# Optimization experiments

Hardware: AMD Instinct MI355X
Metric: run time of the kernel (lower is better)

## Reference

```python
import jax, jax.numpy as jnp
import numpy as np

T = 512          # tokens
H = 2048         # hidden_size
E = 256          # n_routed_experts (8 groups x 32)
G = 8            # tucker groups
EPG = 32         # experts per group
K = 6            # top_k
I = 1408         # moe_intermediate_size
R1 = 128         # tucker input rank
R2 = 128         # tucker output rank


def setup_inputs() -> dict:
    key = jax.random.key(0)
    ks = jax.random.split(key, 12)
    s = 0.02
    return {
        "hidden_states": jax.random.normal(ks[0], (T, H), jnp.float32),
        "w_router": jax.random.normal(ks[1], (H, E), jnp.float32) * s,
        # gate_proj Tucker factors: H -> I
        "U_in_gate": jax.random.normal(ks[2], (G, H, R1), jnp.float32) * s,
        "core_gate": jax.random.normal(ks[3], (E, R1, R2), jnp.float32) * s,
        "U_out_gate": jax.random.normal(ks[4], (G, I, R2), jnp.float32) * s,
        # up_proj Tucker factors: H -> I
        "U_in_up": jax.random.normal(ks[5], (G, H, R1), jnp.float32) * s,
        "core_up": jax.random.normal(ks[6], (E, R1, R2), jnp.float32) * s,
        "U_out_up": jax.random.normal(ks[7], (G, I, R2), jnp.float32) * s,
        # down_proj Tucker factors: I -> H
        "U_in_down": jax.random.normal(ks[8], (G, I, R1), jnp.float32) * s,
        "core_down": jax.random.normal(ks[9], (E, R1, R2), jnp.float32) * s,
        "U_out_down": jax.random.normal(ks[10], (G, H, R2), jnp.float32) * s,
    }


def _tucker_apply(x, g, e, U_in, core, U_out):
    """Per-expert Tucker linear: y_t = ((x_t @ U_in[g_t]) @ core[e_t]) @ U_out[g_t].T
    x: [Td, din]; g: [Td] group ids; e: [Td] full expert ids.
    U_in: [G, din, r1]; core: [E, r1, r2]; U_out: [G, dout, r2]."""
    h1 = jnp.einsum('td,gdr->tgr', x, U_in)                       # [Td, G, r1]
    h1 = jnp.take_along_axis(h1, g[:, None, None], axis=1)[:, 0]  # [Td, r1]
    h2 = jnp.einsum('tr,trs->ts', h1, core[e])                    # [Td, r2]
    y = jnp.einsum('ts,gds->tgd', h2, U_out)                      # [Td, G, dout]
    return jnp.take_along_axis(y, g[:, None, None], axis=1)[:, 0]


def reference(hidden_states, w_router, U_in_gate, core_gate, U_out_gate,
              U_in_up, core_up, U_out_up, U_in_down, core_down, U_out_down):
    n_tok, hid = hidden_states.shape
    router_logits = hidden_states @ w_router                          # [T, E]
    probs = jax.nn.softmax(router_logits.astype(jnp.float32), axis=-1)
    routing_weights, selected = jax.lax.top_k(probs, K)               # [T, K]
    routing_weights = routing_weights / routing_weights.sum(-1, keepdims=True)
    routing_weights = routing_weights.astype(hidden_states.dtype)

    xd = jnp.repeat(hidden_states, K, axis=0)                         # [T*K, H]
    e = selected.reshape(-1)                                          # [T*K]
    g = e // EPG                                                      # group ids

    gate_out = _tucker_apply(xd, g, e, U_in_gate, core_gate, U_out_gate)
    up_out = _tucker_apply(xd, g, e, U_in_up, core_up, U_out_up)
    inter = jax.nn.silu(gate_out) * up_out                            # [T*K, I]
    down_out = _tucker_apply(inter, g, e, U_in_down, core_down, U_out_down)

    combined = (down_out.reshape(n_tok, K, hid) * routing_weights[..., None]).sum(axis=1)
    return combined
```

## Files before the change

### kernel.cpp

```cpp
#include <hip/hip_runtime.h>
#include <cmath>
#include <cstdint>

#define TNUM 512
#define HID 2048
#define NEXP 256
#define NGRP 8
#define KTOP 6
#define IDIM 1408
#define RNK 128
#define NPAIR (TNUM*KTOP)
#define NRCAP 3328
#define MAXTILES (NRCAP/32)

typedef _Float16 f16;
typedef f16  f16x8 __attribute__((ext_vector_type(8)));
typedef f16  f16x4 __attribute__((ext_vector_type(4)));
typedef float f32x4 __attribute__((ext_vector_type(4)));
#define MFMA16(a,b,c) __builtin_amdgcn_mfma_f32_16x16x32_f16((a),(b),(c),0,0,0)

static __device__ __forceinline__ float4 ld4(const float* p){ return *reinterpret_cast<const float4*>(p); }
static __device__ __forceinline__ void st4(float* p, float4 v){ *reinterpret_cast<float4*>(p) = v; }
static __device__ __forceinline__ f16x8 ldh8(const f16* p){ return *reinterpret_cast<const f16x8*>(p); }

constexpr size_t A256(size_t x){ return (x + 255) & ~(size_t)255; }
constexpr size_t OFF_SEL    = 0;
constexpr size_t OFF_WT     = A256(OFF_SEL    + (size_t)NPAIR*4);
constexpr size_t OFF_CNT    = A256(OFF_WT     + (size_t)NPAIR*4);
constexpr size_t OFF_ESTART = A256(OFF_CNT    + (size_t)NEXP*4);
constexpr size_t OFF_TG     = A256(OFF_ESTART + (size_t)NEXP*4);
constexpr size_t OFF_HDR    = A256(OFF_TG     + (size_t)MAXTILES*4);
constexpr size_t OFF_ROWT   = A256(OFF_HDR    + 16);
constexpr size_t OFF_POS    = A256(OFF_ROWT   + (size_t)NRCAP*4);
constexpr size_t OFF_BIG    = A256(OFF_POS    + (size_t)NPAIR*4);

constexpr size_t SZ_XH    = (size_t)TNUM*HID*2;
constexpr size_t SZ_UTI   = (size_t)NGRP*RNK*HID*2;
constexpr size_t SZ_H1ALL = (size_t)2*TNUM*NGRP*RNK*2;
constexpr size_t SZ_UO    = (size_t)NGRP*IDIM*RNK*2;
constexpr size_t SZ_UOD   = (size_t)NGRP*HID*RNK*2;
constexpr size_t SZ_WR    = (size_t)NEXP*HID*2;
constexpr size_t SZ_H2    = (size_t)NRCAP*RNK*2;
constexpr size_t SZ_INTER = (size_t)NRCAP*IDIM*2;
constexpr size_t SZ_DOWNO = (size_t)NRCAP*HID*2;

constexpr size_t OFF_XH    = OFF_BIG;
constexpr size_t OFF_XL    = OFF_XH   + SZ_XH;
constexpr size_t OFF_UTIG  = OFF_XL   + SZ_XH;
constexpr size_t OFF_UTIU  = OFF_UTIG + SZ_UTI;
constexpr size_t OFF_H1    = OFF_UTIU + SZ_UTI;
constexpr size_t REG_END   = OFF_H1   + SZ_H1ALL;
constexpr size_t OFF_INTER = OFF_XH;
constexpr size_t OFF_DOWNO = OFF_XH;
constexpr size_t OFF_LPART = OFF_H1;
constexpr size_t OFF_UOG   = REG_END;
constexpr size_t OFF_UOU   = OFF_UOG  + SZ_UO;
constexpr size_t OFF_UTID  = OFF_UOU  + SZ_UO;
constexpr size_t OFF_UOD   = OFF_UTID + SZ_UO;
constexpr size_t OFF_WRH   = OFF_UOD  + SZ_UOD;
constexpr size_t OFF_WRL   = OFF_WRH  + SZ_WR;
constexpr size_t OFF_H2G   = OFF_WRL  + SZ_WR;
constexpr size_t OFF_H2U   = OFF_H2G  + SZ_H2;
constexpr size_t OFF_D1    = OFF_H2U  + SZ_H2;
constexpr size_t OFF_D2    = OFF_D1   + SZ_H2;
constexpr size_t WS_NEED   = OFF_D2   + SZ_H2;
static_assert(OFF_INTER + SZ_INTER <= OFF_H1 + 0*SZ_H1ALL + (OFF_H1-OFF_XH), "inter overlay");
static_assert(OFF_INTER + SZ_INTER <= OFF_UTIU + SZ_UTI, "inter must end before H1");
static_assert(OFF_DOWNO + SZ_DOWNO <= OFF_UOG, "downo overlay must end before persistent tail");

__global__ __launch_bounds__(256) void k_cvt(
    const float* __restrict__ x,   const float* __restrict__ Uog,
    const float* __restrict__ Uou, const float* __restrict__ Uod,
    const float* __restrict__ wr,
    const float* __restrict__ Uig, const float* __restrict__ Uiu, const float* __restrict__ Uid,
    f16* __restrict__ xh, f16* __restrict__ xl,
    f16* __restrict__ uog, f16* __restrict__ uou, f16* __restrict__ uod,
    f16* __restrict__ wh, f16* __restrict__ wl,
    f16* __restrict__ ig, f16* __restrict__ iu, f16* __restrict__ idn,
    int* __restrict__ cnt){
  __shared__ float tile[32][33];
  const int b = blockIdx.x, tid = threadIdx.x;
  if(b < 1024){
    const size_t i = (size_t)b*256 + tid;
    float4 v = ld4(x + i*4);
    f16x4 H, L;
    H[0]=(f16)v.x; L[0]=(f16)(v.x-(float)H[0]);
    H[1]=(f16)v.y; L[1]=(f16)(v.y-(float)H[1]);
    H[2]=(f16)v.z; L[2]=(f16)(v.z-(float)H[2]);
    H[3]=(f16)v.w; L[3]=(f16)(v.w-(float)H[3]);
    *reinterpret_cast<f16x4*>(xh + i*4) = H;
    *reinterpret_cast<f16x4*>(xl + i*4) = L;
    return;
  }
  if(b < 5888){
    const float* in; f16* hi; size_t i;
    if(b < 2432){        in = Uog; hi = uog; i = (size_t)(b-1024)*256 + tid; }
    else if(b < 3840){   in = Uou; hi = uou; i = (size_t)(b-2432)*256 + tid; }
    else {               in = Uod; hi = uod; i = (size_t)(b-3840)*256 + tid; }
    float4 v = ld4(in + i*4);
    f16x4 H;
    H[0]=(f16)(v.x*16.f); H[1]=(f16)(v.y*16.f); H[2]=(f16)(v.z*16.f); H[3]=(f16)(v.w*16.f);
    *reinterpret_cast<f16x4*>(hi + i*4) = H;
    return;
  }
  if(b < 6400){
    const int wb = b - 5888;
    if(wb == 0) cnt[tid] = 0;
    const int c0 = (wb & 7)*32, r0 = (wb >> 3)*32;
    { const int r = tid>>3, c4 = (tid&7)*4;
      float4 v = ld4(wr + (size_t)(r0+r)*NEXP + c0 + c4);
      tile[r][c4]=v.x; tile[r][c4+1]=v.y; tile[r][c4+2]=v.z; tile[r][c4+3]=v.w; }
    __syncthreads();
    { const int c = tid>>3, r4 = (tid&7)*4;
      f16x4 H, L;
      #pragma unroll
      for(int k = 0; k < 4; k++){
        float v = tile[r4+k][c]*16.f;
        H[k] = (f16)v; L[k] = (f16)(v - (float)H[k]);
      }
      const size_t o = (size_t)(c0+c)*HID + r0 + r4;
      *reinterpret_cast<f16x4*>(wh + o) = H;
      *reinterpret_cast<f16x4*>(wl + o) = L; }
    return;
  }
  const int b2 = b - 6400;
  const int cx = b2 & 3, ry = (b2>>2) & 63, z = b2 >> 8;
  const int tensor = z >> 3, g = z & 7;
  const float* in; f16* o; int R;
  if(tensor == 0){ in = Uig; o = ig; R = HID; }
  else if(tensor == 1){ in = Uiu; o = iu; R = HID; }
  else { in = Uid; o = idn; R = IDIM; }
  const int r0 = ry*32, c0 = cx*32;
  if(r0 >= R) return;
  in += (size_t)g*R*RNK; o += (size_t)g*RNK*R;
  { const int r = tid>>3, c4 = (tid&7)*4;
    float4 v = ld4(in + (size_t)(r0+r)*RNK + c0 + c4);
    tile[r][c4]=v.x; tile[r][c4+1]=v.y; tile[r][c4+2]=v.z; tile[r][c4+3]=v.w; }
  __syncthreads();
  { const int c = tid>>3, r4 = (tid&7)*4;
    f16x4 H;
    #pragma unroll
    for(int k = 0; k < 4; k++) H[k] = (f16)(tile[r4+k][c]*16.f);
    *reinterpret_cast<f16x4*>(o + (size_t)(c0+c)*R + r0 + r4) = H; }
}

__global__ __launch_bounds__(256) void k_router_mfma(
    const f16* __restrict__ xh, const f16* __restrict__ xl,
    const f16* __restrict__ wh, const f16* __restrict__ wl,
    float* __restrict__ lpart){
  __shared__ float red[4][32][64];
  const int m = blockIdx.x, ecol = blockIdx.y, kz = blockIdx.z;
  const int tid = threadIdx.x;
  const int wid = tid>>6, lane = tid&63, q = lane>>4, id = lane&15;
  const int r0 = m*32, e0 = ecol*64;
  const int kb = kz*512 + wid*128;
  f32x4 acc[2][4];
  #pragma unroll
  for(int f = 0; f < 2; f++)
    #pragma unroll
    for(int c = 0; c < 4; c++) acc[f][c] = (f32x4){0.f,0.f,0.f,0.f};
  #pragma unroll
  for(int kk = 0; kk < 128; kk += 32){
    const size_t a0 = (size_t)(r0+id)*HID    + kb + kk + q*8;
    const size_t a1 = (size_t)(r0+16+id)*HID + kb + kk + q*8;
    f16x8 ah0 = ldh8(xh + a0), al0 = ldh8(xl + a0);
    f16x8 ah1 = ldh8(xh + a1), al1 = ldh8(xl + a1);
    #pragma unroll
    for(int c = 0; c < 4; c++){
      const size_t bo = (size_t)(e0 + c*16 + id)*HID + kb + kk + q*8;
      f16x8 bh = ldh8(wh + bo);
      f16x8 bl = ldh8(wl + bo);
      acc[0][c] = MFMA16(ah0, bh, acc[0][c]);
      acc[0][c] = MFMA16(ah0, bl, acc[0][c]);
      acc[0][c] = MFMA16(al0, bh, acc[0][c]);
      acc[1][c] = MFMA16(ah1, bh, acc[1][c]);
      acc[1][c] = MFMA16(ah1, bl, acc[1][c]);
      acc[1][c] = MFMA16(al1, bh, acc[1][c]);
    }
  }
  #pragma unroll
  for(int f = 0; f < 2; f++)
    #pragma unroll
    for(int c = 0; c < 4; c++)
      #pragma unroll
      for(int r = 0; r < 4; r++)
        red[wid][f*16 + q*4 + r][c*16 + id] = acc[f][c][r];
  __syncthreads();
  const int row = tid>>3, c8 = (tid&7)*8;
  float o[8];
  #pragma unroll
  for(int j = 0; j < 8; j++)
    o[j] = (red[0][row][c8+j] + red[1][row][c8+j] + red[2][row][c8+j] + red[3][row][c8+j])*0.0625f;
  float* dst = &lpart[((size_t)kz*TNUM + r0 + row)*NEXP + e0 + c8];
  st4(dst,     make_float4(o[0],o[1],o[2],o[3]));
  st4(dst + 4, make_float4(o[4],o[5],o[6],o[7]));
}

__global__ __launch_bounds__(256) void k_topk(const float* __restrict__ lpart,
                                              int* __restrict__ sel,
                                              float* __restrict__ wt,
                                              int* __restrict__ cnt){
  __shared__ float wv[4];
  __shared__ int   wi[4];
  __shared__ float swin[KTOP];
  __shared__ int   iwin[KTOP];
  const int t = blockIdx.x, tid = threadIdx.x;
  const int lane = tid & 63, wid = tid >> 6;
  const size_t base = (size_t)t*NEXP + tid;
  float v = lpart[base] + lpart[base + (size_t)TNUM*NEXP]
          + lpart[base + (size_t)2*TNUM*NEXP] + lpart[base + (size_t)3*TNUM*NEXP];
  for(int k = 0; k < KTOP; k++){
    float cv = v; int ci = tid;
    #pragma unroll
    for(int off = 1; off < 64; off <<= 1){
      float ov = __shfl_xor(cv, off);
      int   oi = __shfl_xor(ci, off);
      if(ov > cv || (ov == cv && oi < ci)){ cv = ov; ci = oi; }
    }
    if(lane == 0){ wv[wid] = cv; wi[wid] = ci; }
    __syncthreads();
    if(tid == 0){
      float bv = wv[0]; int bi = wi[0];
      #pragma unroll
      for(int w2 = 1; w2 < 4; w2++)
        if(wv[w2] > bv || (wv[w2] == bv && wi[w2] < bi)){ bv = wv[w2]; bi = wi[w2]; }
      swin[k] = bv; iwin[k] = bi;
    }
    __syncthreads();
    if(tid == iwin[k]) v = -INFINITY;
  }
  if(tid == 0){
    float mx = swin[0], s = 0.f, ww[KTOP];
    #pragma unroll
    for(int k = 0; k < KTOP; k++){ ww[k] = expf(swin[k]-mx); s += ww[k]; }
    float inv = 1.f/s;
    #pragma unroll
    for(int k = 0; k < KTOP; k++){
      sel[t*KTOP+k] = iwin[k];
      wt[t*KTOP+k]  = ww[k]*inv;
      atomicAdd(&cnt[iwin[k]], 1);
    }
  }
}

__global__ __launch_bounds__(256) void k_meta_scatter(
    const int* __restrict__ cnt, const int* __restrict__ sel,
    int* __restrict__ estart, int* __restrict__ tile_group, int* __restrict__ hdr,
    int* __restrict__ row_t, int* __restrict__ pos_of_pair){
  __shared__ int scnt[256];
  __shared__ int gsum[8];
  __shared__ int g0[9];
  __shared__ int curs[256];
  const int tid = threadIdx.x;
  scnt[tid] = cnt[tid];
  if(tid < 8) gsum[tid] = 0;
  __syncthreads();
  atomicAdd(&gsum[tid>>5], scnt[tid]);
  __syncthreads();
  if(tid == 0){
    int run = 0;
    for(int g = 0; g < 8; g++){ g0[g] = run; run += (gsum[g]+31) & ~31; }
    g0[8] = run; hdr[0] = run>>5; hdr[1] = run;
  }
  __syncthreads();
  int g = tid >> 5, s = g0[g];
  for(int i = (g<<5); i < tid; i++) s += scnt[i];
  estart[tid] = s; curs[tid] = s;
  const int nt = g0[8] >> 5;
  for(int t2 = tid; t2 < MAXTILES; t2 += 256){
    int gg = -1;
    if(t2 < nt){
      for(int g2 = 0; g2 < 8; g2++) if(t2*32 >= g0[g2] && t2*32 < g0[g2+1]) gg = g2;
    }
    tile_group[t2] = gg;
  }
  __syncthreads();
  for(int p = tid; p < NPAIR; p += 256){
    const int e = sel[p];
    const int pos = atomicAdd(&curs[e], 1);
    row_t[pos] = p / KTOP;
    pos_of_pair[p] = pos;
  }
}

__global__ __launch_bounds__(256) void k_mm_stage1(
    const f16* __restrict__ xh,
    const f16* __restrict__ Bg_, const f16* __restrict__ Bu_,
    f16* __restrict__ H1){
  __shared__ float red[4][32][64];
  const int nt = blockIdx.x, m = blockIdx.y;
  const int pu = nt>>4, g = (nt>>1)&7, ch = nt&1;
  const f16* B = (pu ? Bu_ : Bg_) + (size_t)g*RNK*HID + (size_t)ch*64*HID;
  const int tid = threadIdx.x;
  const int wid = tid>>6, lane = tid&63, q = lane>>4, id = lane&15;
  const int kb = wid*512;
  const int r0 = m*32;
  f32x4 acc[2][4];
  #pragma unroll
  for(int f = 0; f < 2; f++)
    #pragma unroll
    for(int c = 0; c < 4; c++) acc[f][c] = (f32x4){0.f,0.f,0.f,0.f};
  #pragma unroll 4
  for(int kk = 0; kk < 512; kk += 32){
    f16x8 a0 = ldh8(xh + (size_t)(r0+id)*HID    + kb + kk + q*8);
    f16x8 a1 = ldh8(xh + (size_t)(r0+16+id)*HID + kb + kk + q*8);
    #pragma unroll
    for(int c = 0; c < 4; c++){
      f16x8 b = ldh8(B + (size_t)(c*16+id)*HID + kb + kk + q*8);
      acc[0][c] = MFMA16(a0, b, acc[0][c]);
      acc[1][c] = MFMA16(a1, b, acc[1][c]);
    }
  }
  #pragma unroll
  for(int f = 0; f < 2; f++)
    #pragma unroll
    for(int c = 0; c < 4; c++)
      #pragma unroll
      for(int r = 0; r < 4; r++)
        red[wid][f*16 + q*4 + r][c*16 + id] = acc[f][c][r];
  __syncthreads();
  f16* out = H1 + (size_t)pu*TNUM*(NGRP*RNK);
  const int row = tid>>3, c8 = (tid&7)*8;
  f16x8 o8;
  #pragma unroll
  for(int j = 0; j < 8; j++)
    o8[j] = (f16)(red[0][row][c8+j] + red[1][row][c8+j] + red[2][row][c8+j] + red[3][row][c8+j]);
  *reinterpret_cast<f16x8*>(&out[(size_t)(r0+row)*(NGRP*RNK) + g*RNK + ch*64 + c8]) = o8;
}

__global__ __launch_bounds__(256) void k_core2(
    const float* __restrict__ Cg, const float* __restrict__ Cu,
    const f16* __restrict__ H1,
    const int* __restrict__ estart, const int* __restrict__ cnt,
    const int* __restrict__ row_t,
    f16* __restrict__ h2g, f16* __restrict__ h2u){
  __shared__ f16 Cs[RNK][RNK+8];
  __shared__ float tile[32][33];
  const int e = blockIdx.x, up = blockIdx.y;
  const int n = cnt[e];
  if(n == 0) return;
  const float* Cf = (up ? Cu : Cg) + (size_t)e*RNK*RNK;
  const int tid = threadIdx.x;
  #pragma unroll 2
  for(int st = 0; st < 16; st++){
    const int R0 = (st>>2)*32, C0 = (st&3)*32;
    { const int r = tid>>3, c4 = (tid&7)*4;
      float4 v = ld4(Cf + (size_t)(R0+r)*RNK + C0 + c4);
      tile[r][c4]=v.x; tile[r][c4+1]=v.y; tile[r][c4+2]=v.z; tile[r][c4+3]=v.w; }
    __syncthreads();
    { const int c = tid>>3, r4 = (tid&7)*4;
      f16x4 H;
      #pragma unroll
      for(int k2 = 0; k2 < 4; k2++) H[k2] = (f16)(tile[r4+k2][c]*16.f);
      *reinterpret_cast<f16x4*>(&Cs[C0+c][R0+r4]) = H; }
    __syncthreads();
  }
  const int j0 = estart[e], g = e >> 5;
  const f16* A = H1 + (size_t)up*TNUM*(NGRP*RNK);
  f16* o = up ? h2u : h2g;
  const int wid = tid>>6, lane = tid&63, q = lane>>4, id = lane&15;
  for(int rt = 0; rt*16 < n; rt++){
    const int jrow = j0 + rt*16 + id;
    const int jj = jrow < j0+n ? jrow : j0;
    const f16* arow = A + (size_t)row_t[jj]*(NGRP*RNK) + g*RNK;
    f32x4 acc0 = (f32x4){0.f,0.f,0.f,0.f};
    f32x4 acc1 = (f32x4){0.f,0.f,0.f,0.f};
    #pragma unroll
    for(int kk = 0; kk < RNK; kk += 32){
      f16x8 a = ldh8(arow + kk + q*8);
      f16x8 b0 = *reinterpret_cast<const f16x8*>(&Cs[wid*32 + id][kk + q*8]);
      f16x8 b1 = *reinterpret_cast<const f16x8*>(&Cs[wid*32 + 16 + id][kk + q*8]);
      acc0 = MFMA16(a, b0, acc0);
      acc1 = MFMA16(a, b1, acc1);
    }
    #pragma unroll
    for(int r = 0; r < 4; r++){
      const int j = j0 + rt*16 + q*4 + r;
      if(j < j0+n){
        o[(size_t)j*RNK + wid*32 + id]      = (f16)acc0[r];
        o[(size_t)j*RNK + wid*32 + 16 + id] = (f16)acc1[r];
      }
    }
  }
}

__global__ __launch_bounds__(128) void k_mm_gateup(
    const f16* __restrict__ Ag, const f16* __restrict__ Au,
    const f16* __restrict__ Bg, const f16* __restrict__ Bu,
    const int* __restrict__ tg,
    f16* __restrict__ inter){
  const int g = tg[blockIdx.x];
  if(g < 0) return;
  const int j0 = blockIdx.x*32;
  const int tid = threadIdx.x;
  const int wid = tid>>6, lane = tid&63, q = lane>>4, id = lane&15;
  const int c0 = blockIdx.y*128 + wid*64;
  const size_t bbase = (size_t)g*IDIM*RNK;
  f32x4 accg[2][4], accu[2][4];
  #pragma unroll
  for(int f = 0; f < 2; f++)
    #pragma unroll
    for(int c = 0; c < 4; c++){ accg[f][c] = (f32x4){0.f,0.f,0.f,0.f}; accu[f][c] = (f32x4){0.f,0.f,0.f,0.f}; }
  #pragma unroll 2
  for(int kk = 0; kk < RNK; kk += 32){
    const size_t a0off = (size_t)(j0+id)*RNK    + kk + q*8;
    const size_t a1off = (size_t)(j0+16+id)*RNK + kk + q*8;
    f16x8 ag0 = ldh8(Ag + a0off), ag1 = ldh8(Ag + a1off);
    f16x8 au0 = ldh8(Au + a0off), au1 = ldh8(Au + a1off);
    #pragma unroll
    for(int c = 0; c < 4; c++){
      const size_t boff = bbase + (size_t)(c0 + c*16 + id)*RNK + kk + q*8;
      f16x8 bg = ldh8(Bg + boff);
      f16x8 bu = ldh8(Bu + boff);
      accg[0][c] = MFMA16(ag0, bg, accg[0][c]);
      accg[1][c] = MFMA16(ag1, bg, accg[1][c]);
      accu[0][c] = MFMA16(au0, bu, accu[0][c]);
      accu[1][c] = MFMA16(au1, bu, accu[1][c]);
    }
  }
  #pragma unroll
  for(int f = 0; f < 2; f++)
    #pragma unroll
    for(int c = 0; c < 4; c++)
      #pragma unroll
      for(int r = 0; r < 4; r++){
        float vg = accg[f][c][r] * (1.f/4096.f);
        float vu = accu[f][c][r] * (1.f/4096.f);
        float sv = vg/(1.f+expf(-vg))*vu*256.f;
        inter[(size_t)(j0 + f*16 + q*4 + r)*IDIM + c0 + c*16 + id] = (f16)sv;
      }
}

__global__ __launch_bounds__(256) void k_mm_down_in(
    const f16* __restrict__ A_, const f16* __restrict__ B_,
    const int* __restrict__ tg,
    f16* __restrict__ d1){
  __shared__ float red[4][32][64];
  const int g = tg[blockIdx.x];
  if(g < 0) return;
  const int j0 = blockIdx.x*32;
  const int ch = blockIdx.y;
  const f16* B = B_ + (size_t)g*RNK*IDIM + (size_t)ch*64*IDIM;
  const int tid = threadIdx.x;
  const int wid = tid>>6, lane = tid&63, q = lane>>4, id = lane&15;
  const int kb = wid*352;
  f32x4 acc[2][4];
  #pragma unroll
  for(int f = 0; f < 2; f++)
    #pragma unroll
    for(int c = 0; c < 4; c++) acc[f][c] = (f32x4){0.f,0.f,0.f,0.f};
  #pragma unroll 2
  for(int kk = 0; kk < 352; kk += 32){
    f16x8 a0 = ldh8(A_ + (size_t)(j0+id)*IDIM    + kb + kk + q*8);
    f16x8 a1 = ldh8(A_ + (size_t)(j0+16+id)*IDIM + kb + kk + q*8);
    #pragma unroll
    for(int c = 0; c < 4; c++){
      f16x8 b = ldh8(B + (size_t)(c*16+id)*IDIM + kb + kk + q*8);
      acc[0][c] = MFMA16(a0, b, acc[0][c]);
      acc[1][c] = MFMA16(a1, b, acc[1][c]);
    }
  }
  #pragma unroll
  for(int f = 0; f < 2; f++)
    #pragma unroll
    for(int c = 0; c < 4; c++)
      #pragma unroll
      for(int r = 0; r < 4; r++)
        red[wid][f*16 + q*4 + r][c*16 + id] = acc[f][c][r];
  __syncthreads();
  const int row = tid>>3, c8 = (tid&7)*8;
  f16x8 o8;
  #pragma unroll
  for(int j = 0; j < 8; j++)
    o8[j] = (f16)(red[0][row][c8+j] + red[1][row][c8+j] + red[2][row][c8+j] + red[3][row][c8+j]);
  *reinterpret_cast<f16x8*>(&d1[(size_t)(j0+row)*RNK + ch*64 + c8]) = o8;
}

__global__ __launch_bounds__(256) void k_core_down(
    const float* __restrict__ Cd,
    const f16* __restrict__ d1,
    const int* __restrict__ estart, const int* __restrict__ cnt,
    f16* __restrict__ d2){
  __shared__ f16 Cs[RNK][RNK+8];
  __shared__ float tile[32][33];
  const int e = blockIdx.x;
  const int n = cnt[e];
  if(n == 0) return;
  const float* Cf = Cd + (size_t)e*RNK*RNK;
  const int tid = threadIdx.x;
  #pragma unroll 2
  for(int st = 0; st < 16; st++){
    const int R0 = (st>>2)*32, C0 = (st&3)*32;
    { const int r = tid>>3, c4 = (tid&7)*4;
      float4 v = ld4(Cf + (size_t)(R0+r)*RNK + C0 + c4);
      tile[r][c4]=v.x; tile[r][c4+1]=v.y; tile[r][c4+2]=v.z; tile[r][c4+3]=v.w; }
    __syncthreads();
    { const int c = tid>>3, r4 = (tid&7)*4;
      f16x4 H;
      #pragma unroll
      for(int k2 = 0; k2 < 4; k2++) H[k2] = (f16)(tile[r4+k2][c]*16.f);
      *reinterpret_cast<f16x4*>(&Cs[C0+c][R0+r4]) = H; }
    __syncthreads();
  }
  const int j0 = estart[e];
  const int wid = tid>>6, lane = tid&63, q = lane>>4, id = lane&15;
  for(int rt = 0; rt*16 < n; rt++){
    const int jrow = j0 + rt*16 + id;
    const int jj = jrow < j0+n ? jrow : j0;
    const f16* arow = d1 + (size_t)jj*RNK;
    f32x4 acc0 = (f32x4){0.f,0.f,0.f,0.f};
    f32x4 acc1 = (f32x4){0.f,0.f,0.f,0.f};
    #pragma unroll
    for(int kk = 0; kk < RNK; kk += 32){
      f16x8 a = ldh8(arow + kk + q*8);
      f16x8 b0 = *reinterpret_cast<const f16x8*>(&Cs[wid*32 + id][kk + q*8]);
      f16x8 b1 = *reinterpret_cast<const f16x8*>(&Cs[wid*32 + 16 + id][kk + q*8]);
      acc0 = MFMA16(a, b0, acc0);
      acc1 = MFMA16(a, b1, acc1);
    }
    #pragma unroll
    for(int r = 0; r < 4; r++){
      const int j = j0 + rt*16 + q*4 + r;
      if(j < j0+n){
        d2[(size_t)j*RNK + wid*32 + id]      = (f16)acc0[r];
        d2[(size_t)j*RNK + wid*32 + 16 + id] = (f16)acc1[r];
      }
    }
  }
}

__global__ __launch_bounds__(128) void k_mm_down_out(
    const f16* __restrict__ A_, const f16* __restrict__ B_,
    const int* __restrict__ tg,
    f16* __restrict__ downo){
  const int g = tg[blockIdx.x];
  if(g < 0) return;
  const int j0 = blockIdx.x*32;
  const f16* B = B_ + (size_t)g*HID*RNK;
  const int tid = threadIdx.x;
  const int wid = tid>>6, lane = tid&63, q = lane>>4, id = lane&15;
  const int c0 = blockIdx.y*128 + wid*64;
  f32x4 acc[2][4];
  #pragma unroll
  for(int f = 0; f < 2; f++)
    #pragma unroll
    for(int c = 0; c < 4; c++) acc[f][c] = (f32x4){0.f,0.f,0.f,0.f};
  #pragma unroll 2
  for(int kk = 0; kk < RNK; kk += 32){
    f16x8 a0 = ldh8(A_ + (size_t)(j0+id)*RNK    + kk + q*8);
    f16x8 a1 = ldh8(A_ + (size_t)(j0+16+id)*RNK + kk + q*8);
    #pragma unroll
    for(int c = 0; c < 4; c++){
      f16x8 b = ldh8(B + (size_t)(c0 + c*16 + id)*RNK + kk + q*8);
      acc[0][c] = MFMA16(a0, b, acc[0][c]);
      acc[1][c] = MFMA16(a1, b, acc[1][c]);
    }
  }
  #pragma unroll
  for(int f = 0; f < 2; f++)
    #pragma unroll
    for(int c = 0; c < 4; c++)
      #pragma unroll
      for(int r = 0; r < 4; r++)
        downo[(size_t)(j0 + f*16 + q*4 + r)*HID + c0 + c*16 + id] = (f16)(acc[f][c][r]*(1.f/1024.f));
}

__global__ __launch_bounds__(256) void k_combine(const f16* __restrict__ downo,
                                                 const int* __restrict__ pos_of_pair,
                                                 const float* __restrict__ wt,
                                                 float* __restrict__ out){
  const int idx = blockIdx.x*256 + threadIdx.x;
  const int t  = idx >> 9;
  const int h4 = (idx & 511) << 2;
  float4 acc = make_float4(0.f,0.f,0.f,0.f);
  #pragma unroll
  for(int k = 0; k < KTOP; k++){
    const int p = t*KTOP + k;
    const float w = wt[p]*(1.f/1024.f);
    const int pos = pos_of_pair[p];
    f16x4 v = *reinterpret_cast<const f16x4*>(&downo[(size_t)pos*HID + h4]);
    acc.x += w*(float)v[0]; acc.y += w*(float)v[1];
    acc.z += w*(float)v[2]; acc.w += w*(float)v[3];
  }
  st4(&out[(size_t)t*HID + h4], acc);
}

extern "C" void kernel_launch(void* const* d_in, const int* in_sizes, int n_in,
                              void* d_out, int out_size, void* d_ws, size_t ws_size,
                              hipStream_t stream){
  const float* x   = (const float*)d_in[0];
  const float* wr  = (const float*)d_in[1];
  const float* Uig = (const float*)d_in[2];
  const float* cg  = (const float*)d_in[3];
  const float* Uog = (const float*)d_in[4];
  const float* Uiu = (const float*)d_in[5];
  const float* cu  = (const float*)d_in[6];
  const float* Uou = (const float*)d_in[7];
  const float* Uid = (const float*)d_in[8];
  const float* cd  = (const float*)d_in[9];
  const float* Uod = (const float*)d_in[10];
  float* out = (float*)d_out;
  char* ws = (char*)d_ws;
  if(ws_size < WS_NEED) return;

  int*   sel    = (int*)  (ws + OFF_SEL);
  float* wt     = (float*)(ws + OFF_WT);
  int*   cnt    = (int*)  (ws + OFF_CNT);
  int*   estart = (int*)  (ws + OFF_ESTART);
  int*   tg     = (int*)  (ws + OFF_TG);
  int*   hdr    = (int*)  (ws + OFF_HDR);
  int*   row_t  = (int*)  (ws + OFF_ROWT);
  int*   pos    = (int*)  (ws + OFF_POS);
  float* lpart  = (float*)(ws + OFF_LPART);
  f16* xh    = (f16*)(ws + OFF_XH);
  f16* xl    = (f16*)(ws + OFF_XL);
  f16* utig  = (f16*)(ws + OFF_UTIG);
  f16* utiu  = (f16*)(ws + OFF_UTIU);
  f16* H1    = (f16*)(ws + OFF_H1);
  f16* uog   = (f16*)(ws + OFF_UOG);
  f16* uou   = (f16*)(ws + OFF_UOU);
  f16* utid  = (f16*)(ws + OFF_UTID);
  f16* uod   = (f16*)(ws + OFF_UOD);
  f16* wrh   = (f16*)(ws + OFF_WRH);
  f16* wrl   = (f16*)(ws + OFF_WRL);
  f16* h2g   = (f16*)(ws + OFF_H2G);
  f16* h2u   = (f16*)(ws + OFF_H2U);
  f16* inter = (f16*)(ws + OFF_INTER);
  f16* d1    = (f16*)(ws + OFF_D1);
  f16* d2    = (f16*)(ws + OFF_D2);
  f16* downo = (f16*)(ws + OFF_DOWNO);

  k_cvt      <<<12544,             256, 0, stream>>>(x, Uog, Uou, Uod, wr, Uig, Uiu, Uid,
                                                     xh, xl, uog, uou, uod, wrh, wrl,
                                                     utig, utiu, utid, cnt);

  k_router_mfma<<<dim3(16,4,4),    256, 0, stream>>>(xh, xl, wrh, wrl, lpart);
  k_topk     <<<TNUM,              256, 0, stream>>>(lpart, sel, wt, cnt);
  k_meta_scatter<<<1,              256, 0, stream>>>(cnt, sel, estart, tg, hdr, row_t, pos);

  k_mm_stage1<<<dim3(32,16),       256, 0, stream>>>(xh, utig, utiu, H1);
  k_core2    <<<dim3(NEXP,2),      256, 0, stream>>>(cg, cu, H1, estart, cnt, row_t, h2g, h2u);
  k_mm_gateup<<<dim3(MAXTILES,11), 128, 0, stream>>>(h2g, h2u, uog, uou, tg, inter);
  k_mm_down_in<<<dim3(MAXTILES,2), 256, 0, stream>>>(inter, utid, tg, d1);
  k_core_down<<<NEXP,              256, 0, stream>>>(cd, d1, estart, cnt, d2);
  k_mm_down_out<<<dim3(MAXTILES,16),128,0, stream>>>(d2, uod, tg, downo);
  k_combine  <<<1024,              256, 0, stream>>>(downo, pos, wt, out);
}
```

Baseline: 145.6 us.

## Fuse gate/up projection with down-input projection via shared-memory intermediate

Merges the gate/up output projection with SiLU and the down-input projection into one kernel. Each block computes a 352-wide slice of the intermediate into LDS and multiplies it straight into a partial down-input result, so the full intermediate never goes to global memory. Four split-K partial buffers are written, and the core-down kernel sums them in fp16 when it loads them. This drops one launch and the intermediate round trip, but adds partial-sum traffic and fp16 accumulation error, and leaves each block with fewer waves doing the first GEMM.

Result: faster. 136.7 us (median of 2 runs) (-6.1%).

```diff
diff --git a/kernel.cpp b/kernel.cpp
--- a/kernel.cpp
+++ b/kernel.cpp
@@ -41,7 +41,6 @@
 constexpr size_t SZ_UOD   = (size_t)NGRP*HID*RNK*2;
 constexpr size_t SZ_WR    = (size_t)NEXP*HID*2;
 constexpr size_t SZ_H2    = (size_t)NRCAP*RNK*2;
-constexpr size_t SZ_INTER = (size_t)NRCAP*IDIM*2;
 constexpr size_t SZ_DOWNO = (size_t)NRCAP*HID*2;
 
 constexpr size_t OFF_XH    = OFF_BIG;
@@ -50,7 +49,6 @@
 constexpr size_t OFF_UTIU  = OFF_UTIG + SZ_UTI;
 constexpr size_t OFF_H1    = OFF_UTIU + SZ_UTI;
 constexpr size_t REG_END   = OFF_H1   + SZ_H1ALL;
-constexpr size_t OFF_INTER = OFF_XH;
 constexpr size_t OFF_DOWNO = OFF_XH;
 constexpr size_t OFF_LPART = OFF_H1;
 constexpr size_t OFF_UOG   = REG_END;
@@ -61,11 +59,9 @@
 constexpr size_t OFF_WRL   = OFF_WRH  + SZ_WR;
 constexpr size_t OFF_H2G   = OFF_WRL  + SZ_WR;
 constexpr size_t OFF_H2U   = OFF_H2G  + SZ_H2;
-constexpr size_t OFF_D1    = OFF_H2U  + SZ_H2;
-constexpr size_t OFF_D2    = OFF_D1   + SZ_H2;
+constexpr size_t OFF_D1P   = OFF_H2U  + SZ_H2;
+constexpr size_t OFF_D2    = OFF_D1P  + 4*SZ_H2;
 constexpr size_t WS_NEED   = OFF_D2   + SZ_H2;
-static_assert(OFF_INTER + SZ_INTER <= OFF_H1 + 0*SZ_H1ALL + (OFF_H1-OFF_XH), "inter overlay");
-static_assert(OFF_INTER + SZ_INTER <= OFF_UTIU + SZ_UTI, "inter must end before H1");
 static_assert(OFF_DOWNO + SZ_DOWNO <= OFF_UOG, "downo overlay must end before persistent tail");
 
 __global__ __launch_bounds__(256) void k_cvt(
@@ -384,101 +380,82 @@
   }
 }
 
-__global__ __launch_bounds__(128) void k_mm_gateup(
+__global__ __launch_bounds__(256) void k_gateup_downin(
     const f16* __restrict__ Ag, const f16* __restrict__ Au,
     const f16* __restrict__ Bg, const f16* __restrict__ Bu,
+    const f16* __restrict__ Bd,
     const int* __restrict__ tg,
-    f16* __restrict__ inter){
+    f16* __restrict__ d1p){
+  __shared__ f16 inter_s[32][360];
   const int g = tg[blockIdx.x];
   if(g < 0) return;
-  const int j0 = blockIdx.x*32;
-  const int tid = threadIdx.x;
-  const int wid = tid>>6, lane = tid&63, q = lane>>4, id = lane&15;
-  const int c0 = blockIdx.y*128 + wid*64;
+  const int j0 = blockIdx.x*32, qz = blockIdx.y;
+  const int cbase = qz*352;
+  const int tid = threadIdx.x, wid = tid>>6, lane = tid&63, q = lane>>4, id = lane&15;
   const size_t bbase = (size_t)g*IDIM*RNK;
-  f32x4 accg[2][4], accu[2][4];
-  #pragma unroll
-  for(int f = 0; f < 2; f++)
-    #pragma unroll
-    for(int c = 0; c < 4; c++){ accg[f][c] = (f32x4){0.f,0.f,0.f,0.f}; accu[f][c] = (f32x4){0.f,0.f,0.f,0.f}; }
-  #pragma unroll 2
-  for(int kk = 0; kk < RNK; kk += 32){
-    const size_t a0off = (size_t)(j0+id)*RNK    + kk + q*8;
-    const size_t a1off = (size_t)(j0+16+id)*RNK + kk + q*8;
-    f16x8 ag0 = ldh8(Ag + a0off), ag1 = ldh8(Ag + a1off);
-    f16x8 au0 = ldh8(Au + a0off), au1 = ldh8(Au + a1off);
-    #pragma unroll
-    for(int c = 0; c < 4; c++){
-      const size_t boff = bbase + (size_t)(c0 + c*16 + id)*RNK + kk + q*8;
-      f16x8 bg = ldh8(Bg + boff);
-      f16x8 bu = ldh8(Bu + boff);
-      accg[0][c] = MFMA16(ag0, bg, accg[0][c]);
-      accg[1][c] = MFMA16(ag1, bg, accg[1][c]);
-      accu[0][c] = MFMA16(au0, bu, accu[0][c]);
-      accu[1][c] = MFMA16(au1, bu, accu[1][c]);
-    }
-  }
-  #pragma unroll
-  for(int f = 0; f < 2; f++)
-    #pragma unroll
-    for(int c = 0; c < 4; c++)
-      #pragma unroll
-      for(int r = 0; r < 4; r++){
-        float vg = accg[f][c][r] * (1.f/4096.f);
-        float vu = accu[f][c][r] * (1.f/4096.f);
-        float sv = vg/(1.f+expf(-vg))*vu*256.f;
-        inter[(size_t)(j0 + f*16 + q*4 + r)*IDIM + c0 + c*16 + id] = (f16)sv;
-      }
-}
-
-__global__ __launch_bounds__(256) void k_mm_down_in(
-    const f16* __restrict__ A_, const f16* __restrict__ B_,
-    const int* __restrict__ tg,
-    f16* __restrict__ d1){
-  __shared__ float red[4][32][64];
-  const int g = tg[blockIdx.x];
-  if(g < 0) return;
-  const int j0 = blockIdx.x*32;
-  const int ch = blockIdx.y;
-  const f16* B = B_ + (size_t)g*RNK*IDIM + (size_t)ch*64*IDIM;
-  const int tid = threadIdx.x;
-  const int wid = tid>>6, lane = tid&63, q = lane>>4, id = lane&15;
-  const int kb = wid*352;
-  f32x4 acc[2][4];
-  #pragma unroll
-  for(int f = 0; f < 2; f++)
-    #pragma unroll
-    for(int c = 0; c < 4; c++) acc[f][c] = (f32x4){0.f,0.f,0.f,0.f};
+  f16x8 aG[2][4], aU[2][4];
+  #pragma unroll
+  for(int f = 0; f < 2; f++)
+    #pragma unroll
+    for(int k4 = 0; k4 < 4; k4++){
+      const size_t off = (size_t)(j0 + f*16 + id)*RNK + k4*32 + q*8;
+      aG[f][k4] = ldh8(Ag + off);
+      aU[f][k4] = ldh8(Au + off);
+    }
+  for(int t = wid; t < 22; t += 4){
+    const int c0 = cbase + t*16;
+    f32x4 accg0 = (f32x4){0.f,0.f,0.f,0.f}, accg1 = (f32x4){0.f,0.f,0.f,0.f};
+    f32x4 accu0 = (f32x4){0.f,0.f,0.f,0.f}, accu1 = (f32x4){0.f,0.f,0.f,0.f};
+    #pragma unroll
+    for(int k4 = 0; k4 < 4; k4++){
+      const size_t bo = bbase + (size_t)(c0 + id)*RNK + k4*32 + q*8;
+      f16x8 bg = ldh8(Bg + bo);
+      f16x8 bu = ldh8(Bu + bo);
+      accg0 = MFMA16(aG[0][k4], bg, accg0);
+      accg1 = MFMA16(aG[1][k4], bg, accg1);
+      accu0 = MFMA16(aU[0][k4], bu, accu0);
+      accu1 = MFMA16(aU[1][k4], bu, accu1);
+    }
+    #pragma unroll
+    for(int r = 0; r < 4; r++){
+      float vg0 = accg0[r]*(1.f/4096.f), vu0 = accu0[r]*(1.f/4096.f);
+      float vg1 = accg1[r]*(1.f/4096.f), vu1 = accu1[r]*(1.f/4096.f);
+      inter_s[q*4+r][t*16+id]    = (f16)(vg0/(1.f+expf(-vg0))*vu0*256.f);
+      inter_s[16+q*4+r][t*16+id] = (f16)(vg1/(1.f+expf(-vg1))*vu1*256.f);
+    }
+  }
+  __syncthreads();
+  const int col0 = wid*32;
+  f32x4 acc[2][2];
+  #pragma unroll
+  for(int f = 0; f < 2; f++)
+    #pragma unroll
+    for(int c = 0; c < 2; c++) acc[f][c] = (f32x4){0.f,0.f,0.f,0.f};
+  const f16* Bdg = Bd + (size_t)g*RNK*IDIM;
   #pragma unroll 2
   for(int kk = 0; kk < 352; kk += 32){
-    f16x8 a0 = ldh8(A_ + (size_t)(j0+id)*IDIM    + kb + kk + q*8);
-    f16x8 a1 = ldh8(A_ + (size_t)(j0+16+id)*IDIM + kb + kk + q*8);
-    #pragma unroll
-    for(int c = 0; c < 4; c++){
-      f16x8 b = ldh8(B + (size_t)(c*16+id)*IDIM + kb + kk + q*8);
+    f16x8 a0 = *reinterpret_cast<const f16x8*>(&inter_s[id][kk + q*8]);
+    f16x8 a1 = *reinterpret_cast<const f16x8*>(&inter_s[16+id][kk + q*8]);
+    #pragma unroll
+    for(int c = 0; c < 2; c++){
+      f16x8 b = ldh8(Bdg + (size_t)(col0 + c*16 + id)*IDIM + cbase + kk + q*8);
       acc[0][c] = MFMA16(a0, b, acc[0][c]);
       acc[1][c] = MFMA16(a1, b, acc[1][c]);
     }
   }
-  #pragma unroll
-  for(int f = 0; f < 2; f++)
-    #pragma unroll
-    for(int c = 0; c < 4; c++)
+  f16* out = d1p + (size_t)qz*NRCAP*RNK;
+  #pragma unroll
+  for(int f = 0; f < 2; f++)
+    #pragma unroll
+    for(int c = 0; c < 2; c++)
       #pragma unroll
       for(int r = 0; r < 4; r++)
-        red[wid][f*16 + q*4 + r][c*16 + id] = acc[f][c][r];
-  __syncthreads();
-  const int row = tid>>3, c8 = (tid&7)*8;
-  f16x8 o8;
-  #pragma unroll
-  for(int j = 0; j < 8; j++)
-    o8[j] = (f16)(red[0][row][c8+j] + red[1][row][c8+j] + red[2][row][c8+j] + red[3][row][c8+j]);
-  *reinterpret_cast<f16x8*>(&d1[(size_t)(j0+row)*RNK + ch*64 + c8]) = o8;
+        out[(size_t)(j0 + f*16 + q*4 + r)*RNK + col0 + c*16 + id] = (f16)acc[f][c][r];
 }
 
 __global__ __launch_bounds__(256) void k_core_down(
     const float* __restrict__ Cd,
-    const f16* __restrict__ d1,
+    const f16* __restrict__ d1p,
     const int* __restrict__ estart, const int* __restrict__ cnt,
     f16* __restrict__ d2){
   __shared__ f16 Cs[RNK][RNK+8];
@@ -503,16 +480,21 @@
     __syncthreads();
   }
   const int j0 = estart[e];
+  const size_t PL = (size_t)NRCAP*RNK;
   const int wid = tid>>6, lane = tid&63, q = lane>>4, id = lane&15;
   for(int rt = 0; rt*16 < n; rt++){
     const int jrow = j0 + rt*16 + id;
     const int jj = jrow < j0+n ? jrow : j0;
-    const f16* arow = d1 + (size_t)jj*RNK;
+    const size_t arow = (size_t)jj*RNK;
     f32x4 acc0 = (f32x4){0.f,0.f,0.f,0.f};
     f32x4 acc1 = (f32x4){0.f,0.f,0.f,0.f};
     #pragma unroll
     for(int kk = 0; kk < RNK; kk += 32){
-      f16x8 a = ldh8(arow + kk + q*8);
+      const size_t off = arow + kk + q*8;
+      f16x8 a = ldh8(d1p + off);
+      a += ldh8(d1p + off + PL);
+      a += ldh8(d1p + off + 2*PL);
+      a += ldh8(d1p + off + 3*PL);
       f16x8 b0 = *reinterpret_cast<const f16x8*>(&Cs[wid*32 + id][kk + q*8]);
       f16x8 b1 = *reinterpret_cast<const f16x8*>(&Cs[wid*32 + 16 + id][kk + q*8]);
       acc0 = MFMA16(a, b0, acc0);
@@ -625,8 +607,7 @@
   f16* wrl   = (f16*)(ws + OFF_WRL);
   f16* h2g   = (f16*)(ws + OFF_H2G);
   f16* h2u   = (f16*)(ws + OFF_H2U);
-  f16* inter = (f16*)(ws + OFF_INTER);
-  f16* d1    = (f16*)(ws + OFF_D1);
+  f16* d1p   = (f16*)(ws + OFF_D1P);
   f16* d2    = (f16*)(ws + OFF_D2);
   f16* downo = (f16*)(ws + OFF_DOWNO);
 
@@ -640,9 +621,8 @@
 
   k_mm_stage1<<<dim3(32,16),       256, 0, stream>>>(xh, utig, utiu, H1);
   k_core2    <<<dim3(NEXP,2),      256, 0, stream>>>(cg, cu, H1, estart, cnt, row_t, h2g, h2u);
-  k_mm_gateup<<<dim3(MAXTILES,11), 128, 0, stream>>>(h2g, h2u, uog, uou, tg, inter);
-  k_mm_down_in<<<dim3(MAXTILES,2), 256, 0, stream>>>(inter, utid, tg, d1);
-  k_core_down<<<NEXP,              256, 0, stream>>>(cd, d1, estart, cnt, d2);
+  k_gateup_downin<<<dim3(MAXTILES,4),256,0, stream>>>(h2g, h2u, uog, uou, utid, tg, d1p);
+  k_core_down<<<NEXP,              256, 0, stream>>>(cd, d1p, estart, cnt, d2);
   k_mm_down_out<<<dim3(MAXTILES,16),128,0, stream>>>(d2, uod, tg, downo);
   k_combine  <<<1024,              256, 0, stream>>>(downo, pos, wt, out);
 }
```
